# Optimization experiments

Measured on AMD Instinct MI355X. Metric: run time of the kernel, lower is better.

The kernel has to match this reference:

```python
import jax, jax.numpy as jnp
import numpy as np

B, Q, K, D, H, HD, HID, ED, CPB, E = 2, 300, 1024, 256, 8, 32, 32, 256, 256, 131072
N = B * Q
EPS = 1e-5


def _ln(x, g, b):
    mu = x.mean(-1, keepdims=True)
    v = ((x - mu) ** 2).mean(-1, keepdims=True)
    return (x - mu) / jnp.sqrt(v + EPS) * g + b


def setup_inputs():
    key = jax.random.key(0)
    ks = jax.random.split(key, 32)
    rn = lambda k, s, sc=0.02: jax.random.normal(k, s, jnp.float32) * sc
    return {
        "nodes": jax.random.normal(ks[0], (N, D), jnp.float32),
        "images": jax.random.normal(ks[1], (B, K, D), jnp.float32),
        "rel_coords": jax.random.normal(ks[2], (B, Q, K, 2), jnp.float32),
        "edge_feats": jax.random.normal(ks[3], (E, ED), jnp.float32),
        "edge_index": jax.random.randint(ks[4], (2, E), 0, N, jnp.int32),
        "images_mask": jnp.zeros((B, K), dtype=bool),
        "ln1_g": jnp.ones((D,)), "ln1_b": jnp.zeros((D,)),
        "ln2_g": jnp.ones((D,)), "ln2_b": jnp.zeros((D,)),
        "ln3_g": jnp.ones((D,)), "ln3_b": jnp.zeros((D,)),
        "Wni": rn(ks[5], (D, HID * H)), "bni": jnp.zeros((HID * H,)),
        "Wnj": rn(ks[6], (D, HID * H)), "bnj": jnp.zeros((HID * H,)),
        "We": rn(ks[7], (ED, HID * H)), "be": jnp.zeros((HID * H,)),
        "attn_proj": jax.random.normal(ks[8], (H, HID), jnp.float32),
        "Wmsg": rn(ks[9], (D + ED, D)), "bmsg": jnp.zeros((D,)),
        "Wg_out": rn(ks[10], (D, D)), "bg_out": jnp.zeros((D,)),
        "Wq": rn(ks[11], (D, D)), "bq": jnp.zeros((D,)),
        "Wkv": rn(ks[12], (D, 2 * D)), "bkv": jnp.zeros((2 * D,)),
        "Wc1": rn(ks[13], (2, CPB), 0.5), "bc1": jnp.zeros((CPB,)),
        "Wc2": rn(ks[14], (CPB, H), 0.1), "bc2": jnp.zeros((H,)),
        "Wc_out": rn(ks[15], (D, D)), "bc_out": jnp.zeros((D,)),
        "Wf1": rn(ks[16], (D, 4 * D)), "bf1": jnp.zeros((4 * D,)),
        "Wf2": rn(ks[17], (4 * D, D)), "bf2": jnp.zeros((D,)),
    }


def reference(nodes, images, rel_coords, edge_feats, edge_index, images_mask,
              ln1_g, ln1_b, ln2_g, ln2_b, ln3_g, ln3_b,
              Wni, bni, Wnj, bnj, We, be, attn_proj, Wmsg, bmsg, Wg_out, bg_out,
              Wq, bq, Wkv, bkv, Wc1, bc1, Wc2, bc2, Wc_out, bc_out,
              Wf1, bf1, Wf2, bf2):
    src, dst = edge_index[0], edge_index[1]
    # --- graph attention (pre-LN residual) ---
    x = _ln(nodes, ln1_g, ln1_b)
    ni, nj = x[src], x[dst]  # [E, D]
    hidden = jax.nn.leaky_relu(
        ni @ Wni + bni + nj @ Wnj + bnj + edge_feats @ We + be, 0.2)
    hidden = hidden.reshape(E, H, HID)
    logits = jnp.einsum('ehd,hd->eh', hidden, attn_proj)  # [E, H]
    m = jax.ops.segment_max(logits, src, num_segments=N)
    z = jnp.exp(logits - m[src])
    scores = z / jax.ops.segment_sum(z, src, num_segments=N)[src]  # scatter softmax
    msg = (jnp.concatenate([nj, edge_feats], -1) @ Wmsg + bmsg).reshape(E, H, HD)
    agg = jax.ops.segment_sum(msg * scores[..., None], src, num_segments=N).reshape(N, D)
    nodes = nodes + (agg @ Wg_out + bg_out)
    # --- cross attention with continuous position bias ---
    x2 = _ln(nodes, ln2_g, ln2_b).reshape(B, Q, D)
    q = (x2 @ Wq + bq).reshape(B, Q, H, HD).transpose(0, 2, 1, 3)  # [B,H,Q,hd]
    kv = (images @ Wkv + bkv).reshape(B, K, 2, H, HD)
    k = kv[:, :, 0].transpose(0, 2, 1, 3)  # [B,H,K,hd]
    v = kv[:, :, 1].transpose(0, 2, 1, 3)
    cpb = jax.nn.relu(rel_coords @ Wc1 + bc1) @ Wc2 + bc2  # [B,Q,K,H]
    bias = jnp.where(images_mask[:, None, None, :], -jnp.inf,
                     jnp.transpose(cpb, (0, 3, 1, 2)))  # [B,H,Q,K]
    att = jnp.einsum('bhqd,bhkd->bhqk', q, k) / jnp.sqrt(jnp.float32(HD)) + bias
    p = jax.nn.softmax(att, axis=-1)
    out = jnp.einsum('bhqk,bhkd->bhqd', p, v)
    out = out.reshape(B, Q, H * HD)  # faithful to original: reshape WITHOUT head transpose
    nodes = nodes + (out @ Wc_out + bc_out).reshape(N, D)
    # --- FFN (residual from the normed input, as in original) ---
    x3 = _ln(nodes, ln3_g, ln3_b)
    ff = jax.nn.gelu(x3 @ Wf1 + bf1, approximate=False) @ Wf2 + bf2
    return ff + x3
```

## Files before the change

### kernel.cpp

```cpp
#include <hip/hip_runtime.h>
#include <hip/hip_bf16.h>
#include <math.h>

#define E_   131072
#define N_   600
#define NB_  2
#define NQ_  300
#define NK_  1024
#define NH_  8

typedef __hip_bfloat16 bf16;
typedef __bf16 bh8 __attribute__((ext_vector_type(8)));
typedef float  fx4 __attribute__((ext_vector_type(4)));

static __device__ __forceinline__ float b2f(bf16 x){ return __bfloat162float(x); }
static __device__ __forceinline__ unsigned short bfu(float x){
  return __bfloat16_as_ushort(__float2bfloat16(x));
}
static __device__ __forceinline__ unsigned pack2(float x, float y){
  return (unsigned)bfu(x) | ((unsigned)bfu(y) << 16);
}
static __device__ __forceinline__ float ldf(const void* p, size_t i, bool isf32){
  return isf32 ? ((const float*)p)[i] : b2f(((const bf16*)p)[i]);
}

constexpr int WOFF[32] = {
  0,256,512,768,1024,1280,
  1536,67072,67328,132864,
  133120,133376,
  133632,264704,
  264960,330496,330752,396288,
  396544,527616,
  528128,528640,528896,530944,
  530952,596488,
  596744,858888,859912,1122056,
  1122312,
  1187848};
#define NWSEG 31
#define WTOT  1187848
struct SrcTab { const void* p[NWSEG]; };
struct TrTab { int4 d[8]; };

static __device__ __forceinline__ void ln_stats(float v, int t, float* r1, float* r2,
                                                float& mu, float& rstd){
  float s1 = v, s2 = v*v;
  #pragma unroll
  for (int o = 32; o; o >>= 1){ s1 += __shfl_down(s1, o); s2 += __shfl_down(s2, o); }
  if ((t & 63) == 0){ r1[t>>6] = s1; r2[t>>6] = s2; }
  __syncthreads();
  float t1 = r1[0]+r1[1]+r1[2]+r1[3];
  float t2 = r2[0]+r2[1]+r2[2]+r2[3];
  mu = t1 * (1.f/256.f);
  float var = t2 * (1.f/256.f) - mu*mu;
  rstd = rsqrtf(var + 1e-5f);
  __syncthreads();
}

__global__ void k_init(int* cnt, float* denom, const void* nodes, int* dflag){
  int i = blockIdx.x*256 + threadIdx.x;
  if (i < N_) cnt[i] = 0;
  if (i < N_*NH_) denom[i] = 0.f;
  if (i == 0){
    const unsigned short* h = (const unsigned short*)nodes;
    int odd = 0;
    for (int j = 0; j < 64; j++){
      int e = (h[j] >> 7) & 0xFF;
      if (e < 100 || e > 150) odd++;
    }
    *dflag = (odd > 8) ? 1 : 0;
  }
}

__global__ __launch_bounds__(256) void k_cvt(SrcTab tab, float* wall, const int* dflag){
  int i = blockIdx.x*256 + threadIdx.x;
  if (i >= WTOT) return;
  bool isf32 = (*dflag != 0);
  int seg = 0;
  while (seg < NWSEG-1 && i >= WOFF[seg+1]) seg++;
  wall[i] = ldf(tab.p[seg], (size_t)(i - WOFF[seg]), isf32);
}

__global__ __launch_bounds__(256) void k_tr(TrTab tab, const float* __restrict__ wall,
                                            bf16* __restrict__ wbt)
{
  __shared__ float tile[64][65];
  int4 d = tab.d[blockIdx.z];
  int K = d.y, Nn = d.z;
  int k0 = blockIdx.x*64, n0 = blockIdx.y*64;
  if (k0 >= K || n0 >= Nn) return;
  const float* src = wall + d.x;
  bf16* dst = wbt + d.w;
  int t = threadIdx.x;
  int rr = t >> 6, cc = t & 63;
  #pragma unroll
  for (int p = 0; p < 16; p++){
    int row = p*4 + rr;
    tile[row][cc] = src[(size_t)(k0 + row)*Nn + n0 + cc];
  }
  __syncthreads();
  #pragma unroll
  for (int p = 0; p < 16; p++){
    int row = p*4 + rr;
    dst[(size_t)(n0 + row)*K + k0 + cc] = __float2bfloat16(tile[cc][row]);
  }
}

__global__ __launch_bounds__(256) void k_ln1(
    const void* __restrict__ nodes, const int* __restrict__ dflag,
    const float* __restrict__ g1, const float* __restrict__ b1, bf16* __restrict__ x1)
{
  __shared__ float r1[4], r2[4];
  int n = blockIdx.x, t = threadIdx.x;
  bool isf32 = (*dflag != 0);
  float v = ldf(nodes, (size_t)n*256 + t, isf32);
  float mu, rstd;
  ln_stats(v, t, r1, r2, mu, rstd);
  x1[n*256 + t] = __float2bfloat16((v - mu) * rstd * g1[t] + b1[t]);
}

__global__ void k_count(const int* __restrict__ ei, int* cnt){
  int e = blockIdx.x*256 + threadIdx.x;
  atomicAdd(&cnt[ei[e]], 1);
}

__global__ __launch_bounds__(1024) void k_scan(const int* __restrict__ cnt,
                                               int* offs, int* cursor){
  __shared__ int s[1024];
  int t = threadIdx.x;
  s[t] = (t < N_) ? cnt[t] : 0;
  __syncthreads();
  for (int o = 1; o < 1024; o <<= 1){
    int v = 0;
    if (t >= o) v = s[t - o];
    __syncthreads();
    if (t >= o) s[t] += v;
    __syncthreads();
  }
  if (t < N_){ int excl = (t == 0) ? 0 : s[t-1]; offs[t] = excl; cursor[t] = excl; }
  if (t == N_-1) offs[N_] = s[N_-1];
}

__global__ void k_scatter(const int* __restrict__ ei, int* cursor, int* eorder){
  int e = blockIdx.x*256 + threadIdx.x;
  int pos = atomicAdd(&cursor[ei[e]], 1);
  eorder[pos] = e;
}

__global__ __launch_bounds__(256) void k_gemm_dual(
    const void* __restrict__ A, int m_base, const int* __restrict__ dflag,
    const bf16* __restrict__ BT, bf16* __restrict__ C)
{
  __shared__ __align__(16) bf16 As[128*40];
  __shared__ __align__(16) bf16 Bs[128*40];
  int m0 = blockIdx.x * 128;
  int n0 = blockIdx.y * 128;
  int t = threadIdx.x;
  bool isf32 = (*dflag != 0);
  int wave = t >> 6, lane = t & 63;
  int wr = (wave >> 1) * 64, wc = (wave & 1) * 64;
  int lm = lane & 15, lq = lane >> 4;
  int srow = t >> 2;
  int scol = (t & 3) * 8;
  size_t r0 = (size_t)(m_base + m0 + srow) * 256;
  size_t r1 = (size_t)(m_base + m0 + 64 + srow) * 256;
  fx4 acc[4][4] = {};
  for (int kk = 0; kk < 256; kk += 32){
    uint4 pa0, pa1;
    if (isf32){
      const float* a0p = (const float*)A + r0 + kk + scol;
      const float* a1p = (const float*)A + r1 + kk + scol;
      float4 va0a = *(const float4*)(a0p);
      float4 va0b = *(const float4*)(a0p + 4);
      float4 va1a = *(const float4*)(a1p);
      float4 va1b = *(const float4*)(a1p + 4);
      pa0.x = pack2(va0a.x, va0a.y); pa0.y = pack2(va0a.z, va0a.w);
      pa0.z = pack2(va0b.x, va0b.y); pa0.w = pack2(va0b.z, va0b.w);
      pa1.x = pack2(va1a.x, va1a.y); pa1.y = pack2(va1a.z, va1a.w);
      pa1.z = pack2(va1b.x, va1b.y); pa1.w = pack2(va1b.z, va1b.w);
    } else {
      pa0 = *(const uint4*)((const bf16*)A + r0 + kk + scol);
      pa1 = *(const uint4*)((const bf16*)A + r1 + kk + scol);
    }
    float4 vb0 = *(const float4*)(BT + (size_t)(n0 + srow)      * 256 + kk + scol);
    float4 vb1 = *(const float4*)(BT + (size_t)(n0 + 64 + srow) * 256 + kk + scol);
    __syncthreads();
    *(uint4*)(As + srow*40 + scol)         = pa0;
    *(uint4*)(As + (64 + srow)*40 + scol)  = pa1;
    *(float4*)(Bs + srow*40 + scol)        = vb0;
    *(float4*)(Bs + (64 + srow)*40 + scol) = vb1;
    __syncthreads();
    bh8 af[4], bfr[4];
    #pragma unroll
    for (int mt = 0; mt < 4; mt++)
      af[mt] = *reinterpret_cast<const bh8*>(As + (wr + mt*16 + lm)*40 + lq*8);
    #pragma unroll
    for (int nt = 0; nt < 4; nt++)
      bfr[nt] = *reinterpret_cast<const bh8*>(Bs + (wc + nt*16 + lm)*40 + lq*8);
    #pragma unroll
    for (int mt = 0; mt < 4; mt++)
      #pragma unroll
      for (int nt = 0; nt < 4; nt++)
        acc[mt][nt] = __builtin_amdgcn_mfma_f32_16x16x32_bf16(af[mt], bfr[nt], acc[mt][nt], 0, 0, 0);
  }
  #pragma unroll
  for (int mt = 0; mt < 4; mt++)
    #pragma unroll
    for (int nt = 0; nt < 4; nt++)
      #pragma unroll
      for (int r = 0; r < 4; r++){
        int row = m0 + wr + mt*16 + lq*4 + r;
        int col = n0 + wc + nt*16 + lm;
        C[(size_t)row*256 + col] = __float2bfloat16(acc[mt][nt][r]);
      }
}

__global__ __launch_bounds__(256) void k_gemm(
    const void* __restrict__ A, const int* __restrict__ dflag, int adual,
    int K, int M, const bf16* __restrict__ BT, int mode,
    void* __restrict__ D, int ldd,
    const float* __restrict__ bias, const float* __restrict__ add,
    float* __restrict__ aux)
{
  __shared__ __align__(16) bf16 As[128*40];
  __shared__ __align__(16) bf16 Bs[128*40];
  int m0 = blockIdx.x * 128;
  int n0 = blockIdx.y * 128;
  int t = threadIdx.x;
  bool f32src = adual && (*dflag != 0);
  int wave = t >> 6, lane = t & 63;
  int wr = (wave >> 1) * 64, wc = (wave & 1) * 64;
  int lm = lane & 15, lq = lane >> 4;
  int srow = t >> 2;
  int scol = (t & 3) * 8;
  size_t rA0 = (size_t)(m0 + srow) * K;
  size_t rA1 = (size_t)(m0 + 64 + srow) * K;
  size_t rB0 = (size_t)(n0 + srow) * K;
  size_t rB1 = (size_t)(n0 + 64 + srow) * K;
  fx4 acc[4][4] = {};
  for (int kk = 0; kk < K; kk += 32){
    uint4 pa0, pa1;
    if (f32src){
      const float* a0p = (const float*)A + rA0 + kk + scol;
      const float* a1p = (const float*)A + rA1 + kk + scol;
      float4 a = *(const float4*)(a0p), b = *(const float4*)(a0p + 4);
      float4 c = *(const float4*)(a1p), d = *(const float4*)(a1p + 4);
      pa0.x = pack2(a.x,a.y); pa0.y = pack2(a.z,a.w);
      pa0.z = pack2(b.x,b.y); pa0.w = pack2(b.z,b.w);
      pa1.x = pack2(c.x,c.y); pa1.y = pack2(c.z,c.w);
      pa1.z = pack2(d.x,d.y); pa1.w = pack2(d.z,d.w);
    } else {
      pa0 = *(const uint4*)((const bf16*)A + rA0 + kk + scol);
      pa1 = *(const uint4*)((const bf16*)A + rA1 + kk + scol);
    }
    float4 vb0 = *(const float4*)(BT + rB0 + kk + scol);
    float4 vb1 = *(const float4*)(BT + rB1 + kk + scol);
    __syncthreads();
    *(uint4*)(As + srow*40 + scol)         = pa0;
    *(uint4*)(As + (64 + srow)*40 + scol)  = pa1;
    *(float4*)(Bs + srow*40 + scol)        = vb0;
    *(float4*)(Bs + (64 + srow)*40 + scol) = vb1;
    __syncthreads();
    bh8 af[4], bfr[4];
    #pragma unroll
    for (int mt = 0; mt < 4; mt++)
      af[mt] = *reinterpret_cast<const bh8*>(As + (wr + mt*16 + lm)*40 + lq*8);
    #pragma unroll
    for (int nt = 0; nt < 4; nt++)
      bfr[nt] = *reinterpret_cast<const bh8*>(Bs + (wc + nt*16 + lm)*40 + lq*8);
    #pragma unroll
    for (int mt = 0; mt < 4; mt++)
      #pragma unroll
      for (int nt = 0; nt < 4; nt++)
        acc[mt][nt] = __builtin_amdgcn_mfma_f32_16x16x32_bf16(af[mt], bfr[nt], acc[mt][nt], 0, 0, 0);
  }
  #pragma unroll
  for (int mt = 0; mt < 4; mt++)
    #pragma unroll
    for (int nt = 0; nt < 4; nt++)
      #pragma unroll
      for (int r = 0; r < 4; r++){
        int row = m0 + wr + mt*16 + lq*4 + r;
        int col = n0 + wc + nt*16 + lm;
        if (row >= M) continue;
        float v = acc[mt][nt][r];
        if (mode == 0){
          if (bias) v += bias[col];
          ((float*)D)[(size_t)row*ldd + col] = v;
        } else if (mode == 1){
          v += bias[col];
          if (col < 256){
            ((float*)D)[(size_t)row*256 + col] = v;
          } else {
            int b = row >> 10, ki = row & 1023;
            int hh = (col - 256) >> 5, dd = (col - 256) & 31;
            aux[(((size_t)b*NH_ + hh)*32 + dd)*NK_ + ki] = v;
          }
        } else if (mode == 2){
          v += bias[col] + add[(size_t)row*ldd + col];
          ((float*)D)[(size_t)row*ldd + col] = v;
        } else {
          v += bias[col];
          float g = 0.5f*v*(1.f + erff(v*0.70710678118654752f));
          ((bf16*)D)[(size_t)row*ldd + col] = __float2bfloat16(g);
        }
      }
}

__global__ __launch_bounds__(256) void k_logits(
    const bf16* __restrict__ He, const float* __restrict__ Pall,
    const float* __restrict__ bni, const float* __restrict__ bnj, const float* __restrict__ be,
    const float* __restrict__ ap, const int* __restrict__ ei,
    float* __restrict__ z, float* __restrict__ denom, int e0chunk)
{
  __shared__ float hs[32*264];
  __shared__ int   ssh[32], dsh[32];
  __shared__ float aps[256], bhs[256];
  int t = threadIdx.x;
  int base = e0chunk + blockIdx.x*32;
  if (t < 32) ssh[t] = ei[base + t];
  else if (t < 64) dsh[t-32] = ei[E_ + base + (t - 32)];
  aps[t] = ap[t];
  bhs[t] = bni[t] + bnj[t] + be[t];
  __syncthreads();
  int slot = (t >> 5)*33 + (t & 31);
  for (int r = 0; r < 32; r++){
    float v = b2f(He[(size_t)(base - e0chunk + r)*256 + t])
            + Pall[ssh[r]*768 + t] + Pall[dsh[r]*768 + 256 + t] + bhs[t];
    v = (v > 0.f) ? v : 0.2f*v;
    hs[r*264 + slot] = v;
  }
  __syncthreads();
  int e = t >> 3, h = t & 7;
  const float* hr  = hs + e*264 + h*33;
  const float* apr = aps + h*32;
  float acc = 0.f;
  #pragma unroll
  for (int i = 0; i < 32; i++) acc = fmaf(hr[i], apr[i], acc);
  float zv = __expf(fminf(acc, 30.f));
  z[(size_t)(base + e)*8 + h] = zv;
  atomicAdd(&denom[ssh[e]*8 + h], zv);
}

__global__ __launch_bounds__(256) void k_agg_e(
    const int* __restrict__ offs, const int* __restrict__ eorder, const int* __restrict__ ei,
    const float* __restrict__ z,
    const void* __restrict__ ef, const int* __restrict__ dflag,
    const float* __restrict__ Pall,
    float* __restrict__ Fbuf, float* __restrict__ Gbuf)
{
  __shared__ float zsh[32*8];
  __shared__ int   esh[32];
  __shared__ int   dsh[32];
  int n = blockIdx.x, s = blockIdx.y, t = threadIdx.x;
  bool isf32 = (*dflag != 0);
  int h = t >> 5;
  int e0 = offs[n], e1 = offs[n+1];
  int total = e1 - e0;
  int quarter = (total + 3) >> 2;
  int start = e0 + s*quarter;
  int end   = min(e1, start + quarter);
  float facc[8] = {};
  float gacc = 0.f;
  int jz = t >> 3, hz = t & 7;
  for (int base = start; base < end; base += 32){
    int cnt = min(32, end - base);
    __syncthreads();
    if (t < 32){
      int e = (t < cnt) ? eorder[base + t] : eorder[start];
      esh[t] = e;
      dsh[t] = ei[E_ + e];
    }
    __syncthreads();
    zsh[t] = (jz < cnt) ? z[(size_t)esh[jz]*8 + hz] : 0.f;
    __syncthreads();
    #pragma unroll 8
    for (int jj = 0; jj < 32; jj++){
      int e = esh[jj];
      float efv = ldf(ef, (size_t)e*256 + t, isf32);
      float pv  = Pall[(size_t)dsh[jj]*768 + 512 + t];
      #pragma unroll
      for (int hq = 0; hq < 8; hq++) facc[hq] = fmaf(zsh[jj*8 + hq], efv, facc[hq]);
      gacc = fmaf(zsh[jj*8 + h], pv, gacc);
    }
  }
  int slot = n*4 + s;
  #pragma unroll
  for (int hq = 0; hq < 8; hq++)
    Fbuf[((size_t)slot*8 + hq)*256 + t] = facc[hq];
  Gbuf[(size_t)slot*256 + t] = gacc;
}

__global__ __launch_bounds__(256) void k_agg_n(
    const float* __restrict__ Fbuf, const float* __restrict__ Gbuf,
    const float* __restrict__ denom,
    const float* __restrict__ bmsg, const float* __restrict__ Wmsg,
    const void* __restrict__ nodes, const int* __restrict__ dflag,
    const float* __restrict__ Wg, const float* __restrict__ bg,
    const float* __restrict__ g2, const float* __restrict__ b2v,
    const float* __restrict__ Wq, const float* __restrict__ bq,
    float* __restrict__ nodes1, float* __restrict__ qbuf)
{
  __shared__ float sinv[8];
  __shared__ float Fs[8*257];
  __shared__ float aggs[256];
  __shared__ float r1[4], r2[4];
  int n = blockIdx.x, t = threadIdx.x;
  bool isf32 = (*dflag != 0);
  int h = t >> 5;
  if (t < 8){
    float dsum = denom[n*8 + t];
    sinv[t] = (dsum > 0.f) ? 1.f/dsum : 0.f;
  }
  __syncthreads();
  #pragma unroll
  for (int hq = 0; hq < 8; hq++){
    float f = 0.f;
    #pragma unroll
    for (int s = 0; s < 4; s++)
      f += Fbuf[((size_t)(n*4 + s)*8 + hq)*256 + t];
    Fs[hq*257 + t] = f * sinv[hq];
  }
  float gacc = 0.f;
  #pragma unroll
  for (int s = 0; s < 4; s++) gacc += Gbuf[(size_t)(n*4 + s)*256 + t];
  gacc *= sinv[h];
  __syncthreads();
  float am = gacc + bmsg[t];
  const float* fr = Fs + h*257;
  for (int k = 0; k < 256; k++)
    am = fmaf(fr[k], Wmsg[(size_t)(256 + k)*256 + t], am);
  aggs[t] = am;
  __syncthreads();
  float o = bg[t] + ldf(nodes, (size_t)n*256 + t, isf32);
  for (int k = 0; k < 256; k++) o = fmaf(aggs[k], Wg[k*256 + t], o);
  nodes1[n*256 + t] = o;
  float mu, rstd;
  ln_stats(o, t, r1, r2, mu, rstd);
  float x2 = (o - mu) * rstd * g2[t] + b2v[t];
  __syncthreads();
  aggs[t] = x2;
  __syncthreads();
  float q = bq[t];
  for (int k = 0; k < 256; k++) q = fmaf(aggs[k], Wq[k*256 + t], q);
  qbuf[n*256 + t] = q;
}

__global__ __launch_bounds__(256) void k_cpb(
    const void* __restrict__ rel, const int* __restrict__ dflag,
    const float* __restrict__ Wc1, const float* __restrict__ bc1,
    const float* __restrict__ Wc2, const float* __restrict__ bc2, bf16* __restrict__ bias)
{
  __shared__ float w0[256], w1[256], bb[256], w2[256*8], b2s[8];
  int t = threadIdx.x;
  bool isf32 = (*dflag != 0);
  w0[t] = Wc1[t]; w1[t] = Wc1[256 + t]; bb[t] = bc1[t];
  for (int i = t; i < 2048; i += 256) w2[i] = Wc2[i];
  if (t < 8) b2s[t] = bc2[t];
  __syncthreads();
  size_t pos = (size_t)blockIdx.x*256 + t;
  float c0 = ldf(rel, pos*2, isf32), c1 = ldf(rel, pos*2 + 1, isf32);
  float acc[8] = {};
  for (int j = 0; j < 256; j++){
    float hj = fmaf(c0, w0[j], fmaf(c1, w1[j], bb[j]));
    hj = fmaxf(hj, 0.f);
    #pragma unroll
    for (int h = 0; h < 8; h++) acc[h] = fmaf(hj, w2[j*8 + h], acc[h]);
  }
  int k = (int)(pos & 1023);
  size_t qq = pos >> 10;
  size_t b = qq / NQ_, q = qq % NQ_;
  bf16* dst = bias + ((b*NH_)*NQ_ + q)*NK_;
  #pragma unroll
  for (int h = 0; h < 8; h++)
    dst[(size_t)h*NQ_*NK_ + k] = __float2bfloat16(acc[h] + b2s[h]);
}

__global__ __launch_bounds__(256) void k_attn(
    const float* __restrict__ qbuf, const float* __restrict__ kbuf, const float* __restrict__ vT,
    const bf16* __restrict__ bias, bf16* __restrict__ Yb)
{
  __shared__ float Qs[8*33];
  __shared__ float Ks[128*33];
  __shared__ float Sc[8*1024];
  __shared__ float Op[4*8*32];
  __shared__ float qs[8];
  int qt = blockIdx.x, h = blockIdx.y, b = blockIdx.z;
  int q0 = qt*8;
  int t = threadIdx.x;
  {
    int q = t >> 5, d = t & 31;
    int gq = q0 + q;
    Qs[q*33 + d] = (gq < NQ_) ? qbuf[((size_t)b*NQ_ + gq)*256 + h*32 + d] : 0.f;
  }
  const float* kbase = kbuf + (size_t)b*NK_*256 + h*32;
  const bf16*  bb    = bias + ((size_t)(b*NH_ + h)*NQ_)*NK_;
  int kl = t & 127;
  int qb = (t >> 7) * 4;
  for (int kt = 0; kt < 8; kt++){
    int k0 = kt*128;
    __syncthreads();
    {
      int r = t >> 1, c0 = (t & 1) * 16;
      const float* src = kbase + (size_t)(k0 + r)*256 + c0;
      float* dst = Ks + r*33 + c0;
      #pragma unroll
      for (int ii = 0; ii < 4; ii++){
        float4 f = *(const float4*)(src + ii*4);
        dst[ii*4+0]=f.x; dst[ii*4+1]=f.y; dst[ii*4+2]=f.z; dst[ii*4+3]=f.w;
      }
    }
    __syncthreads();
    float a0=0.f, a1=0.f, a2=0.f, a3=0.f;
    const float* kr = Ks + kl*33;
    #pragma unroll
    for (int i = 0; i < 32; i++){
      float kd = kr[i];
      a0 = fmaf(kd, Qs[(qb+0)*33+i], a0);
      a1 = fmaf(kd, Qs[(qb+1)*33+i], a1);
      a2 = fmaf(kd, Qs[(qb+2)*33+i], a2);
      a3 = fmaf(kd, Qs[(qb+3)*33+i], a3);
    }
    float av[4] = {a0,a1,a2,a3};
    #pragma unroll
    for (int j = 0; j < 4; j++){
      int gq = min(q0 + qb + j, NQ_-1);
      float s = av[j]*0.17677669529663689f + b2f(bb[(size_t)gq*NK_ + k0 + kl]);
      Sc[(qb+j)*1024 + k0 + kl] = s;
    }
  }
  __syncthreads();
  {
    int q = t >> 5, j = t & 31;
    float m = -1e30f;
    for (int k = j; k < 1024; k += 32) m = fmaxf(m, Sc[q*1024 + k]);
    #pragma unroll
    for (int o = 16; o; o >>= 1) m = fmaxf(m, __shfl_xor(m, o));
    float ssum = 0.f;
    for (int k = j; k < 1024; k += 32){
      float e = __expf(Sc[q*1024 + k] - m);
      Sc[q*1024 + k] = e;
      ssum += e;
    }
    #pragma unroll
    for (int o = 16; o; o >>= 1) ssum += __shfl_xor(ssum, o);
    if (j == 0) qs[q] = ssum;
  }
  int d = t & 31, qg = (t >> 5) & 1, ks = t >> 6;
  const float* vrb = vT + (((size_t)(b*NH_ + h))*32)*NK_;
  float o0=0.f, o1=0.f, o2=0.f, o3=0.f;
  for (int kt = 0; kt < 8; kt++){
    int k0 = kt*128;
    __syncthreads();
    {
      int d2 = t >> 3, kq = (t & 7) * 16;
      const float* src = vrb + (size_t)d2*NK_ + k0 + kq;
      #pragma unroll
      for (int ii = 0; ii < 4; ii++){
        float4 f = *(const float4*)(src + ii*4);
        Ks[(kq+ii*4+0)*33 + d2] = f.x;
        Ks[(kq+ii*4+1)*33 + d2] = f.y;
        Ks[(kq+ii*4+2)*33 + d2] = f.z;
        Ks[(kq+ii*4+3)*33 + d2] = f.w;
      }
    }
    __syncthreads();
    const float* sc0 = Sc + (qg*4+0)*1024 + k0 + ks*32;
    const float* sc1 = Sc + (qg*4+1)*1024 + k0 + ks*32;
    const float* sc2 = Sc + (qg*4+2)*1024 + k0 + ks*32;
    const float* sc3 = Sc + (qg*4+3)*1024 + k0 + ks*32;
    #pragma unroll
    for (int kk = 0; kk < 32; kk++){
      float vv = Ks[(ks*32+kk)*33 + d];
      o0 = fmaf(sc0[kk], vv, o0);
      o1 = fmaf(sc1[kk], vv, o1);
      o2 = fmaf(sc2[kk], vv, o2);
      o3 = fmaf(sc3[kk], vv, o3);
    }
  }
  Op[((ks*8) + qg*4 + 0)*32 + d] = o0;
  Op[((ks*8) + qg*4 + 1)*32 + d] = o1;
  Op[((ks*8) + qg*4 + 2)*32 + d] = o2;
  Op[((ks*8) + qg*4 + 3)*32 + d] = o3;
  __syncthreads();
  {
    int q = t >> 5, dd = t & 31;
    int gq = q0 + q;
    if (gq < NQ_){
      float s = Op[(0*8+q)*32+dd] + Op[(1*8+q)*32+dd]
              + Op[(2*8+q)*32+dd] + Op[(3*8+q)*32+dd];
      float sv = s / qs[q];
      int tt = h*NQ_ + gq;
      Yb[((size_t)b*NQ_ + (tt >> 3))*256 + (tt & 7)*32 + dd] = __float2bfloat16(sv);
    }
  }
}

__global__ __launch_bounds__(256) void k_ln3(
    const float* __restrict__ n2, const float* __restrict__ g3, const float* __restrict__ b3,
    float* __restrict__ x3f, bf16* __restrict__ x3b)
{
  __shared__ float r1[4], r2[4];
  int n = blockIdx.x, t = threadIdx.x;
  float v = n2[n*256 + t];
  float mu, rstd;
  ln_stats(v, t, r1, r2, mu, rstd);
  float x3 = (v - mu) * rstd * g3[t] + b3[t];
  x3f[n*256 + t] = x3;
  x3b[n*256 + t] = __float2bfloat16(x3);
}

extern "C" void kernel_launch(void* const* d_in, const int* in_sizes, int n_in,
                              void* d_out, int out_size, void* d_ws, size_t ws_size,
                              hipStream_t stream)
{
  const void* nodes  = d_in[0];
  const void* images = d_in[1];
  const void* rel    = d_in[2];
  const void* ef     = d_in[3];
  const int*  ei     = (const int*)d_in[4];
  float* out = (float*)d_out;

  char* w = (char*)d_ws;
  auto alloc = [&](size_t bytes) -> void* {
    void* p = (void*)w; w += (bytes + 255) & ~(size_t)255; return p;
  };
  int*      dflag  = (int*)     alloc(4);
  float*    Wall   = (float*)   alloc((size_t)WTOT*4);
  bf16*     Wbt    = (bf16*)    alloc((size_t)983040*2);
  bf16*     bias   = (bf16*)    alloc((size_t)NB_*NH_*NQ_*NK_*2);
  float*    zbuf   = (float*)   alloc((size_t)E_*8*4);
  float*    Pall   = (float*)   alloc((size_t)N_*768*4);
  float*    Fbuf   = (float*)   alloc((size_t)N_*4*8*256*4);
  float*    Gbuf   = (float*)   alloc((size_t)N_*4*256*4);
  float*    nodes1 = (float*)   alloc(N_*256*4);
  float*    qbuf   = (float*)   alloc(N_*256*4);
  float*    kbuf   = (float*)   alloc((size_t)NB_*NK_*256*4);
  float*    vT     = (float*)   alloc((size_t)NB_*NH_*32*NK_*4);
  float*    n2buf  = (float*)   alloc(N_*256*4);
  float*    x3f    = (float*)   alloc(N_*256*4);
  bf16*     x1     = (bf16*)    alloc(N_*256*2);
  bf16*     x3b    = (bf16*)    alloc(N_*256*2);
  bf16*     Yb     = (bf16*)    alloc(N_*256*2);
  bf16*     H1     = (bf16*)    alloc((size_t)N_*1024*2);
  float*    denom  = (float*)   alloc(N_*8*4);
  int*      cnt    = (int*)     alloc(N_*4);
  int*      offs   = (int*)     alloc((N_+1)*4);
  int*      cursor = (int*)     alloc(N_*4);
  int*      eorder = (int*)     alloc((size_t)E_*4);
  size_t used = (size_t)(w - (char*)d_ws);
  int CH = E_;
  while (CH > 2048 && used + (size_t)CH*256*2 + 256 > ws_size) CH >>= 1;
  bf16* He = (bf16*)alloc((size_t)CH*256*2);

  bf16* WeT  = Wbt + 0;
  bf16* WkvT = Wbt + 65536;
  bf16* WnpT = Wbt + 196608;
  bf16* WcoT = Wbt + 393216;
  bf16* Wf1T = Wbt + 458752;
  bf16* Wf2T = Wbt + 720896;

  const float *ln1g=Wall+WOFF[0],  *ln1b=Wall+WOFF[1];
  const float *ln2g=Wall+WOFF[2],  *ln2b=Wall+WOFF[3];
  const float *ln3g=Wall+WOFF[4],  *ln3b=Wall+WOFF[5];
  const float *bni=Wall+WOFF[7],  *bnj=Wall+WOFF[9], *be=Wall+WOFF[10];
  const float *ap =Wall+WOFF[11];
  const float *Wmsg=Wall+WOFF[12], *bmsg=Wall+WOFF[13];
  const float *Wg=Wall+WOFF[14], *bg=Wall+WOFF[15];
  const float *Wq=Wall+WOFF[16], *bq=Wall+WOFF[17];
  const float *bkv=Wall+WOFF[19];
  const float *Wc1=Wall+WOFF[20], *bc1=Wall+WOFF[21];
  const float *Wc2=Wall+WOFF[22], *bc2=Wall+WOFF[23];
  const float *bco=Wall+WOFF[25];
  const float *bf1v=Wall+WOFF[27];
  const float *bf2v=Wall+WOFF[29];

  SrcTab tab;
  {
    const int idx[NWSEG] = {6,7,8,9,10,11, 12,13,14,15, 17,18, 19,20, 21,22,23,24,
                            25,26, 27,28,29,30, 31,32, 33,34,35,36, 16};
    for (int i = 0; i < NWSEG; i++) tab.p[i] = d_in[idx[i]];
  }
  TrTab tr;
  tr.d[0] = {WOFF[30], 256,  256, 0};
  tr.d[1] = {WOFF[18], 256,  512, 65536};
  tr.d[2] = {WOFF[6],  256,  256, 196608};
  tr.d[3] = {WOFF[8],  256,  256, 196608+65536};
  tr.d[4] = {WOFF[12], 256,  256, 196608+131072};
  tr.d[5] = {WOFF[24], 256,  256, 393216};
  tr.d[6] = {WOFF[26], 256, 1024, 458752};
  tr.d[7] = {WOFF[28],1024,  256, 720896};

  k_init   <<<19, 256, 0, stream>>>(cnt, denom, nodes, dflag);
  k_cvt    <<<(WTOT+255)/256, 256, 0, stream>>>(tab, Wall, dflag);
  k_tr     <<<dim3(16,16,8), 256, 0, stream>>>(tr, Wall, Wbt);
  k_ln1    <<<N_, 256, 0, stream>>>(nodes, dflag, ln1g, ln1b, x1);
  k_count  <<<E_/256, 256, 0, stream>>>(ei, cnt);
  k_scan   <<<1, 1024, 0, stream>>>(cnt, offs, cursor);
  k_scatter<<<E_/256, 256, 0, stream>>>(ei, cursor, eorder);

  k_gemm<<<dim3(5,6), 256, 0, stream>>>(x1, dflag, 0, 256, N_, WnpT, 0,
                                        Pall, 768, nullptr, nullptr, nullptr);

  for (int c0 = 0; c0 < E_; c0 += CH){
    k_gemm_dual<<<dim3(CH/128, 2), 256, 0, stream>>>(ef, c0, dflag, WeT, He);
    k_logits   <<<CH/32, 256, 0, stream>>>(He, Pall, bni, bnj, be, ap, ei,
                                           zbuf, denom, c0);
  }
  k_agg_e  <<<dim3(N_,4), 256, 0, stream>>>(offs, eorder, ei, zbuf, ef, dflag, Pall,
                                            Fbuf, Gbuf);
  k_agg_n  <<<N_, 256, 0, stream>>>(Fbuf, Gbuf, denom, bmsg, Wmsg, nodes, dflag,
                                    Wg, bg, ln2g, ln2b, Wq, bq, nodes1, qbuf);
  k_gemm<<<dim3(16,4), 256, 0, stream>>>(images, dflag, 1, 256, NB_*NK_, WkvT, 1,
                                         kbuf, 256, bkv, nullptr, vT);
  k_cpb    <<<NB_*NQ_*NK_/256, 256, 0, stream>>>(rel, dflag, Wc1, bc1, Wc2, bc2, bias);
  dim3 agrid((NQ_ + 7)/8, NH_, NB_);
  k_attn   <<<agrid, 256, 0, stream>>>(qbuf, kbuf, vT, bias, Yb);
  k_gemm<<<dim3(5,2), 256, 0, stream>>>(Yb, dflag, 0, 256, N_, WcoT, 2,
                                        n2buf, 256, bco, nodes1, nullptr);
  k_ln3  <<<N_, 256, 0, stream>>>(n2buf, ln3g, ln3b, x3f, x3b);
  k_gemm<<<dim3(5,8), 256, 0, stream>>>(x3b, dflag, 0, 256, N_, Wf1T, 3,
                                        H1, 1024, bf1v, nullptr, nullptr);
  k_gemm<<<dim3(5,2), 256, 0, stream>>>(H1, dflag, 0, 1024, N_, Wf2T, 2,
                                        out, 256, bf2v, x3f, nullptr);
}
```

Before: 735.7 us.

## Fuse edge projection GEMM with attention logits epilogue

Merges the per-edge feature GEMM and the logits kernel into one kernel. The epilogue adds the gathered node projections and biases, applies leaky ReLU, dots with attn_proj through a wave-shuffle reduction per head, then writes exp logits and atomically accumulates denominators. This removes the bf16 He intermediate write and re-read (E x 256) and one launch per chunk. In exchange the epilogue does scattered Pall gathers, and the bni/bnj/be shared-memory loads are not explicitly synchronized before use, though the main loop's barriers cover them.

```diff
diff --git a/kernel.cpp b/kernel.cpp
--- a/kernel.cpp
+++ b/kernel.cpp
@@ -146,12 +146,17 @@
   eorder[pos] = e;
 }
 
-__global__ __launch_bounds__(256) void k_gemm_dual(
-    const void* __restrict__ A, int m_base, const int* __restrict__ dflag,
-    const bf16* __restrict__ BT, bf16* __restrict__ C)
+__global__ __launch_bounds__(256) void k_gemm_logits(
+    const void* __restrict__ ef, const int* __restrict__ dflag,
+    const bf16* __restrict__ BT, const float* __restrict__ Pall,
+    const float* __restrict__ bni, const float* __restrict__ bnj, const float* __restrict__ be,
+    const float* __restrict__ ap, const int* __restrict__ ei,
+    float* __restrict__ z, float* __restrict__ denom)
 {
   __shared__ __align__(16) bf16 As[128*40];
   __shared__ __align__(16) bf16 Bs[128*40];
+  __shared__ int   ssh[128], dsh[128];
+  __shared__ float apsh[128], bhsh[128];
   int m0 = blockIdx.x * 128;
   int n0 = blockIdx.y * 128;
   int t = threadIdx.x;
@@ -161,14 +166,22 @@
   int lm = lane & 15, lq = lane >> 4;
   int srow = t >> 2;
   int scol = (t & 3) * 8;
-  size_t r0 = (size_t)(m_base + m0 + srow) * 256;
-  size_t r1 = (size_t)(m_base + m0 + 64 + srow) * 256;
+  if (t < 128){
+    ssh[t] = ei[m0 + t];
+    apsh[t] = ap[n0 + t];
+  } else {
+    int j = t - 128;
+    dsh[j] = ei[E_ + m0 + j];
+    bhsh[j] = bni[n0 + j] + bnj[n0 + j] + be[n0 + j];
+  }
+  size_t r0 = (size_t)(m0 + srow) * 256;
+  size_t r1 = (size_t)(m0 + 64 + srow) * 256;
   fx4 acc[4][4] = {};
   for (int kk = 0; kk < 256; kk += 32){
     uint4 pa0, pa1;
     if (isf32){
-      const float* a0p = (const float*)A + r0 + kk + scol;
-      const float* a1p = (const float*)A + r1 + kk + scol;
+      const float* a0p = (const float*)ef + r0 + kk + scol;
+      const float* a1p = (const float*)ef + r1 + kk + scol;
       float4 va0a = *(const float4*)(a0p);
       float4 va0b = *(const float4*)(a0p + 4);
       float4 va1a = *(const float4*)(a1p);
@@ -178,8 +191,8 @@
       pa1.x = pack2(va1a.x, va1a.y); pa1.y = pack2(va1a.z, va1a.w);
       pa1.z = pack2(va1b.x, va1b.y); pa1.w = pack2(va1b.z, va1b.w);
     } else {
-      pa0 = *(const uint4*)((const bf16*)A + r0 + kk + scol);
-      pa1 = *(const uint4*)((const bf16*)A + r1 + kk + scol);
+      pa0 = *(const uint4*)((const bf16*)ef + r0 + kk + scol);
+      pa1 = *(const uint4*)((const bf16*)ef + r1 + kk + scol);
     }
     float4 vb0 = *(const float4*)(BT + (size_t)(n0 + srow)      * 256 + kk + scol);
     float4 vb1 = *(const float4*)(BT + (size_t)(n0 + 64 + srow) * 256 + kk + scol);
@@ -203,15 +216,39 @@
         acc[mt][nt] = __builtin_amdgcn_mfma_f32_16x16x32_bf16(af[mt], bfr[nt], acc[mt][nt], 0, 0, 0);
   }
   #pragma unroll
-  for (int mt = 0; mt < 4; mt++)
-    #pragma unroll
-    for (int nt = 0; nt < 4; nt++)
+  for (int mt = 0; mt < 4; mt++){
+    float lacc[4][2] = {};
+    #pragma unroll
+    for (int r = 0; r < 4; r++){
+      int row = wr + mt*16 + lq*4 + r;
+      int s = ssh[row], d = dsh[row];
+      const float* ps = Pall + (size_t)s*768;
+      const float* pd = Pall + (size_t)d*768 + 256;
       #pragma unroll
-      for (int r = 0; r < 4; r++){
-        int row = m0 + wr + mt*16 + lq*4 + r;
-        int col = n0 + wc + nt*16 + lm;
-        C[(size_t)row*256 + col] = __float2bfloat16(acc[mt][nt][r]);
+      for (int nt = 0; nt < 4; nt++){
+        int cl = wc + nt*16 + lm;
+        int cg = n0 + cl;
+        float v = acc[mt][nt][r] + ps[cg] + pd[cg] + bhsh[cl];
+        v = (v > 0.f) ? v : 0.2f*v;
+        lacc[r][nt>>1] = fmaf(v, apsh[cl], lacc[r][nt>>1]);
       }
+    }
+    #pragma unroll
+    for (int r = 0; r < 4; r++)
+      #pragma unroll
+      for (int p = 0; p < 2; p++){
+        float v = lacc[r][p];
+        v += __shfl_xor(v, 1); v += __shfl_xor(v, 2);
+        v += __shfl_xor(v, 4); v += __shfl_xor(v, 8);
+        if (lm == 0){
+          int row = wr + mt*16 + lq*4 + r;
+          int h = blockIdx.y*4 + (wc >> 5) + p;
+          float zv = __expf(fminf(v, 30.f));
+          z[(size_t)(m0 + row)*8 + h] = zv;
+          atomicAdd(&denom[ssh[row]*8 + h], zv);
+        }
+      }
+  }
 }
 
 __global__ __launch_bounds__(256) void k_gemm(
@@ -306,41 +343,6 @@
       }
 }
 
-__global__ __launch_bounds__(256) void k_logits(
-    const bf16* __restrict__ He, const float* __restrict__ Pall,
-    const float* __restrict__ bni, const float* __restrict__ bnj, const float* __restrict__ be,
-    const float* __restrict__ ap, const int* __restrict__ ei,
-    float* __restrict__ z, float* __restrict__ denom, int e0chunk)
-{
-  __shared__ float hs[32*264];
-  __shared__ int   ssh[32], dsh[32];
-  __shared__ float aps[256], bhs[256];
-  int t = threadIdx.x;
-  int base = e0chunk + blockIdx.x*32;
-  if (t < 32) ssh[t] = ei[base + t];
-  else if (t < 64) dsh[t-32] = ei[E_ + base + (t - 32)];
-  aps[t] = ap[t];
-  bhs[t] = bni[t] + bnj[t] + be[t];
-  __syncthreads();
-  int slot = (t >> 5)*33 + (t & 31);
-  for (int r = 0; r < 32; r++){
-    float v = b2f(He[(size_t)(base - e0chunk + r)*256 + t])
-            + Pall[ssh[r]*768 + t] + Pall[dsh[r]*768 + 256 + t] + bhs[t];
-    v = (v > 0.f) ? v : 0.2f*v;
-    hs[r*264 + slot] = v;
-  }
-  __syncthreads();
-  int e = t >> 3, h = t & 7;
-  const float* hr  = hs + e*264 + h*33;
-  const float* apr = aps + h*32;
-  float acc = 0.f;
-  #pragma unroll
-  for (int i = 0; i < 32; i++) acc = fmaf(hr[i], apr[i], acc);
-  float zv = __expf(fminf(acc, 30.f));
-  z[(size_t)(base + e)*8 + h] = zv;
-  atomicAdd(&denom[ssh[e]*8 + h], zv);
-}
-
 __global__ __launch_bounds__(256) void k_agg_e(
     const int* __restrict__ offs, const int* __restrict__ eorder, const int* __restrict__ ei,
     const float* __restrict__ z,
@@ -647,10 +649,6 @@
   int*      offs   = (int*)     alloc((N_+1)*4);
   int*      cursor = (int*)     alloc(N_*4);
   int*      eorder = (int*)     alloc((size_t)E_*4);
-  size_t used = (size_t)(w - (char*)d_ws);
-  int CH = E_;
-  while (CH > 2048 && used + (size_t)CH*256*2 + 256 > ws_size) CH >>= 1;
-  bf16* He = (bf16*)alloc((size_t)CH*256*2);
 
   bf16* WeT  = Wbt + 0;
   bf16* WkvT = Wbt + 65536;
@@ -701,11 +699,10 @@
   k_gemm<<<dim3(5,6), 256, 0, stream>>>(x1, dflag, 0, 256, N_, WnpT, 0,
                                         Pall, 768, nullptr, nullptr, nullptr);
 
-  for (int c0 = 0; c0 < E_; c0 += CH){
-    k_gemm_dual<<<dim3(CH/128, 2), 256, 0, stream>>>(ef, c0, dflag, WeT, He);
-    k_logits   <<<CH/32, 256, 0, stream>>>(He, Pall, bni, bnj, be, ap, ei,
-                                           zbuf, denom, c0);
-  }
+  k_gemm_logits<<<dim3(E_/128, 2), 256, 0, stream>>>(ef, dflag, WeT, Pall,
+                                                     bni, bnj, be, ap, ei,
+                                                     zbuf, denom);
+
   k_agg_e  <<<dim3(N_,4), 256, 0, stream>>>(offs, eorder, ei, zbuf, ef, dflag, Pall,
                                             Fbuf, Gbuf);
   k_agg_n  <<<N_, 256, 0, stream>>>(Fbuf, Gbuf, denom, bmsg, Wmsg, nodes, dflag,
```

New measurement: 783.5 us. +6.5%, slower.
